# Optimization experiments

Hardware: AMD Instinct MI355X
Metric: run time of the kernel (lower is better)

The kernel has to match this reference:

```python
import jax, jax.numpy as jnp
import numpy as np

T, B, D_IN, D_H, D_OUT = 16, 8192, 512, 1024, 256


def setup_inputs() -> dict:
    key = jax.random.key(0)
    ks = jax.random.split(key, 4)
    # He-style scaled init to keep activations sane
    x = jax.random.normal(ks[0], (B, D_IN), dtype=jnp.float32)
    W1 = jax.random.normal(ks[1], (T, D_IN, D_H), dtype=jnp.float32) / np.sqrt(D_IN)
    b1 = jnp.zeros((T, D_H), dtype=jnp.float32)
    W2 = jax.random.normal(ks[2], (T, D_H, D_H), dtype=jnp.float32) / np.sqrt(D_H)
    b2 = jnp.zeros((T, D_H), dtype=jnp.float32)
    W3 = jax.random.normal(ks[3], (T, D_H, D_OUT), dtype=jnp.float32) / np.sqrt(D_H)
    b3 = jnp.zeros((T, D_OUT), dtype=jnp.float32)
    return {"x": x, "W1": W1, "b1": b1, "W2": W2, "b2": b2, "W3": W3, "b3": b3}


def reference(x, W1, b1, W2, b2, W3, b3):
    # Batched over the tree dimension t: one grouped GEMM per layer instead of
    # a Python loop over trees.
    h = jax.nn.relu(jnp.einsum('bi,tih->tbh', x, W1) + b1[:, None, :])   # [T,B,H]
    h = jax.nn.relu(jnp.einsum('tbh,thk->tbk', h, W2) + b2[:, None, :])  # [T,B,H]
    out = jnp.einsum('tbh,tho->tbo', h, W3) + b3[:, None, :]             # [T,B,O]
    return jnp.mean(out, axis=0)                                          # [B,O]
```

## Files before the change

### kernel.cpp

```cpp
#include <hip/hip_runtime.h>
#include <hip/hip_bf16.h>
#include <stdint.h>

#define T_TREES 16
#define B_ROWS  8192
#define DIN     512
#define DH      1024
#define DOUT    256

typedef unsigned short u16;
typedef __attribute__((ext_vector_type(8))) short short8;
typedef __attribute__((ext_vector_type(16))) float floatx16;

__device__ __forceinline__ u16 f2bf(float f) {
    union { float f; uint32_t u; } v; v.f = f;
    uint32_t u = v.u;
    uint32_t r = (u + 0x7fffu + ((u >> 16) & 1u)) >> 16;
    return (u16)r;
}

__device__ __forceinline__ void async_copy16(const u16* g, u16* l) {
    __builtin_amdgcn_global_load_lds(
        (const __attribute__((address_space(1))) uint32_t*)g,
        (__attribute__((address_space(3))) uint32_t*)l,
        16, 0, 0);
}

__global__ void prep_v9(const float* __restrict__ x, u16* __restrict__ xb,
                        const float* __restrict__ b3, float* __restrict__ out,
                        const float* __restrict__ W1, const float* __restrict__ W2,
                        const float* __restrict__ W3,
                        u16* __restrict__ W1b, u16* __restrict__ W2b,
                        u16* __restrict__ W3b) {
    __shared__ float tile[32][33];
    if (blockIdx.x < 4096) {
        int idx = blockIdx.x * 256 + threadIdx.x;
        float4 v = ((const float4*)x)[idx];
        ushort4 o;
        o.x = f2bf(v.x); o.y = f2bf(v.y); o.z = f2bf(v.z); o.w = f2bf(v.w);
        ((ushort4*)xb)[idx] = o;
    } else if (blockIdx.x < 12288) {
        int idx = (blockIdx.x - 4096) * 256 + threadIdx.x;
        int o = idx & (DOUT - 1);
        float s = 0.f;
#pragma unroll
        for (int t = 0; t < T_TREES; t++) s += b3[t * DOUT + o];
        out[idx] = s * (1.f / T_TREES);
    } else {
        int bid = blockIdx.x - 12288;
        int t = bid / 1792, tl = bid - t * 1792;
        const float* in; u16* outp; int K, N, kt, nt; float scale = 1.f;
        if (tl < 512)       { in = W1; outp = W1b; K = DIN; N = DH;   kt = tl & 15; nt = tl >> 4; }
        else if (tl < 1536) { tl -= 512;  in = W2; outp = W2b; K = DH; N = DH;   kt = tl & 31; nt = tl >> 5; }
        else                { tl -= 1536; in = W3; outp = W3b; K = DH; N = DOUT; kt = tl & 31; nt = tl >> 5;
                              scale = 1.f / T_TREES; }
        int k0 = kt * 32, n0 = nt * 32;
        const float* inb = in + (size_t)t * K * N;
        u16* outb = outp + (size_t)t * K * N;
        int c4 = threadIdx.x & 7, rr = threadIdx.x >> 3;
        float4 v = *(const float4*)&inb[(size_t)(k0 + rr) * N + n0 + c4 * 4];
        tile[rr][c4 * 4 + 0] = v.x;
        tile[rr][c4 * 4 + 1] = v.y;
        tile[rr][c4 * 4 + 2] = v.z;
        tile[rr][c4 * 4 + 3] = v.w;
        __syncthreads();
        if (threadIdx.x < 128) {
            int n  = threadIdx.x >> 2;
            int kq = threadIdx.x & 3;
            short8 o;
#pragma unroll
            for (int j = 0; j < 8; j++)
                ((u16*)&o)[j] = f2bf(tile[kq * 8 + j][n] * scale);
            *(short8*)&outb[(size_t)(n0 + n) * K + k0 + kq * 8] = o;
        }
    }
}

__global__ void reduce_v9(const float* __restrict__ Part, float* __restrict__ Out, int g) {
    int idx = blockIdx.x * 256 + threadIdx.x;
    float4 s = ((const float4*)Out)[idx];
    for (int t = 0; t < g; t++) {
        float4 p = ((const float4*)(Part + (size_t)t * B_ROWS * DOUT))[idx];
        s.x += p.x; s.y += p.y; s.z += p.z; s.w += p.w;
    }
    ((float4*)Out)[idx] = s;
}


#define GEMM_PREAMBLE_COMMON()                               \
    const int tid  = threadIdx.x;                            \
    const int wave = tid >> 6;                               \
    const int lane = tid & 63;                               \
    const int l31  = lane & 31;                              \
    const int h    = lane >> 5;                              \
    const int rg   = tid >> 3;                               \
    const int colE = (((tid & 7) ^ (rg & 7)) << 3);          \
    const int xm   = l31 & 7;

#define STAGE256(kt_, p_)                                                              \
    {                                                                                  \
        const int k0_ = (kt_) * 64;                                                    \
        u16* lA_ = lds + (p_) * 32768 + wave * 512;                                    \
        u16* lB_ = lA_ + 16384;                                                        \
        _Pragma("unroll")                                                              \
        for (int j_ = 0; j_ < 4; j_++) {                                               \
            const int row_ = j_ * 64 + rg;                                             \
            async_copy16(Ab + (size_t)(m0 + row_) * K + k0_ + colE, lA_ + j_ * 4096);  \
            async_copy16(Bb + (size_t)(n0 + row_) * K + k0_ + colE, lB_ + j_ * 4096);  \
        }                                                                              \
    }

#define C256_PASS(A_, B_, mh_)                                                         \
    {                                                                                  \
        short8 afr[2][4];                                                              \
        _Pragma("unroll")                                                              \
        for (int mf = 0; mf < 2; mf++) {                                               \
            const int r_ = wm2 * 128 + (mh_) * 64 + mf * 32 + l31;                     \
            _Pragma("unroll")                                                          \
            for (int kk = 0; kk < 4; kk++)                                             \
                afr[mf][kk] = *(const short8*)&A_[r_ * 64 + (((kk * 2 + h) ^ xm) << 3)]; \
        }                                                                              \
        __builtin_amdgcn_s_setprio(1);                                                 \
        _Pragma("unroll")                                                              \
        for (int kk = 0; kk < 4; kk++)                                                 \
            _Pragma("unroll")                                                          \
            for (int mf = 0; mf < 2; mf++)                                             \
                _Pragma("unroll")                                                      \
                for (int nf = 0; nf < 2; nf++)                                         \
                    acc[(mh_) * 2 + mf][nf] = __builtin_amdgcn_mfma_f32_32x32x16_bf16( \
                        afr[mf][kk], bfr[nf][kk], acc[(mh_) * 2 + mf][nf], 0, 0, 0);   \
        __builtin_amdgcn_s_setprio(0);                                                 \
    }

#define COMPUTE256(p_)                                                                 \
    {                                                                                  \
        const u16* A_ = lds + (p_) * 32768;                                            \
        const u16* B_ = A_ + 16384;                                                    \
        short8 bfr[2][4];                                                              \
        _Pragma("unroll")                                                              \
        for (int nf = 0; nf < 2; nf++) {                                               \
            const int r_ = wn4 * 64 + nf * 32 + l31;                                   \
            _Pragma("unroll")                                                          \
            for (int kk = 0; kk < 4; kk++)                                             \
                bfr[nf][kk] = *(const short8*)&B_[r_ * 64 + (((kk * 2 + h) ^ xm) << 3)]; \
        }                                                                              \
        if (wm2 == 0) { C256_PASS(A_, B_, 0); C256_PASS(A_, B_, 1); }                  \
        else          { C256_PASS(A_, B_, 1); C256_PASS(A_, B_, 0); }                  \
    }

#define GEMM_MAIN(STAGE_, COMPUTE_)                                              \
    STAGE_(0, 0);                                                                \
    STAGE_(1, 1);                                                                \
    for (int kt = 0; kt < NT; kt++) {                                            \
        const int p_ = kt & 1;                                                   \
        if (kt < NT - 1) asm volatile("s_waitcnt vmcnt(8)\n\ts_barrier" ::: "memory"); \
        else             asm volatile("s_waitcnt vmcnt(0)\n\ts_barrier" ::: "memory"); \
        COMPUTE_(p_);                                                            \
        asm volatile("s_barrier" ::: "memory");                                  \
        if (kt + 2 < NT) STAGE_(kt + 2, p_);                                     \
    }

__global__ __launch_bounds__(512, 2)
void gemm_l2_v9(const u16* __restrict__ A, size_t aStrideT,
                const u16* __restrict__ Bt,
                const float* __restrict__ bias,
                u16* __restrict__ C,
                int M, int N, int K) {
    extern __shared__ u16 lds[];

    const int t = blockIdx.z;
    const u16* Ab = A + (size_t)t * aStrideT;
    const u16* Bb = Bt + (size_t)t * (size_t)N * K;
    u16* Cb = C + (size_t)t * (size_t)M * N;
    const float* biasb = bias + (size_t)t * N;

    const int m0 = blockIdx.x * 256;
    const int n0 = blockIdx.y * 256;

    GEMM_PREAMBLE_COMMON();
    const int wm2 = wave >> 2;
    const int wn4 = wave & 3;

    floatx16 acc[4][2];
#pragma unroll
    for (int ai = 0; ai < 4; ai++)
#pragma unroll
        for (int nf = 0; nf < 2; nf++)
#pragma unroll
            for (int r = 0; r < 16; r++) acc[ai][nf][r] = 0.f;

    const int NT = K >> 6;
    GEMM_MAIN(STAGE256, COMPUTE256);

#pragma unroll
    for (int nf = 0; nf < 2; nf++) {
        const int n = n0 + wn4 * 64 + nf * 32 + l31;
        const float bv = biasb[n];
#pragma unroll
        for (int ai = 0; ai < 4; ai++) {
#pragma unroll
            for (int r = 0; r < 16; r++) {
                const int m = m0 + wm2 * 128 + ai * 32 + (r & 3) + 8 * (r >> 2) + 4 * h;
                float v = acc[ai][nf][r] + bv;
                v = v > 0.f ? v : 0.f;
                Cb[(size_t)m * N + n] = f2bf(v);
            }
        }
    }
}

#define STAGE128(kt_, p_)                                                              \
    {                                                                                  \
        const int k0_ = (kt_) * 64;                                                    \
        u16* lA_ = lds + (p_) * 16384 + wave * 512;                                    \
        u16* lB_ = lA_ + 8192;                                                         \
        _Pragma("unroll")                                                              \
        for (int j_ = 0; j_ < 4; j_++) {                                               \
            const int row_ = j_ * 32 + rg;                                             \
            async_copy16(Ab + (size_t)(m0 + row_) * K + k0_ + colE, lA_ + j_ * 2048);  \
            async_copy16(Bb + (size_t)(n0 + row_) * K + k0_ + colE, lB_ + j_ * 2048);  \
        }                                                                              \
    }

#define STAGE_L3(kt_, p_)                                                              \
    {                                                                                  \
        const int lt_ = ltBase + ((kt_) >> 4);                                         \
        const int k0_ = ((kt_) & 15) * 64;                                             \
        const u16* At_ = H2g + (size_t)lt_ * B_ROWS * DH;                              \
        const u16* Bt_ = W3g + (size_t)lt_ * DOUT * DH;                                \
        u16* lA_ = lds + (p_) * 16384 + wave * 512;                                    \
        u16* lB_ = lA_ + 8192;                                                         \
        _Pragma("unroll")                                                              \
        for (int j_ = 0; j_ < 4; j_++) {                                               \
            const int row_ = j_ * 32 + rg;                                             \
            async_copy16(At_ + (size_t)(m0 + row_) * DH + k0_ + colE, lA_ + j_ * 2048);\
            async_copy16(Bt_ + (size_t)(n0 + row_) * DH + k0_ + colE, lB_ + j_ * 2048);\
        }                                                                              \
    }

#define COMPUTE128(p_)                                                                 \
    {                                                                                  \
        const u16* A_ = lds + (p_) * 16384;                                            \
        const u16* B_ = A_ + 8192;                                                     \
        short8 bfr[2][4], afr[2][4];                                                   \
        _Pragma("unroll")                                                              \
        for (int nf = 0; nf < 2; nf++) {                                               \
            const int r_ = wn + nf * 32 + l31;                                         \
            _Pragma("unroll")                                                          \
            for (int kk = 0; kk < 4; kk++)                                             \
                bfr[nf][kk] = *(const short8*)&B_[r_ * 64 + (((kk * 2 + h) ^ xm) << 3)]; \
        }                                                                              \
        _Pragma("unroll")                                                              \
        for (int mf = 0; mf < 2; mf++) {                                               \
            const int r_ = wm + mf * 32 + l31;                                         \
            _Pragma("unroll")                                                          \
            for (int kk = 0; kk < 4; kk++)                                             \
                afr[mf][kk] = *(const short8*)&A_[r_ * 64 + (((kk * 2 + h) ^ xm) << 3)]; \
        }                                                                              \
        __builtin_amdgcn_s_setprio(1);                                                 \
        _Pragma("unroll")                                                              \
        for (int kk = 0; kk < 4; kk++)                                                 \
            _Pragma("unroll")                                                          \
            for (int mf = 0; mf < 2; mf++)                                             \
                _Pragma("unroll")                                                      \
                for (int nf = 0; nf < 2; nf++)                                         \
                    acc[mf][nf] = __builtin_amdgcn_mfma_f32_32x32x16_bf16(             \
                        afr[mf][kk], bfr[nf][kk], acc[mf][nf], 0, 0, 0);               \
        __builtin_amdgcn_s_setprio(0);                                                 \
    }

__global__ __launch_bounds__(256, 2)
void gemm_l1_v9(const u16* __restrict__ A, size_t aStrideT,
                const u16* __restrict__ Bt,
                const float* __restrict__ bias,
                u16* __restrict__ C,
                int M, int N, int K) {
    extern __shared__ u16 lds[];

    const int t = blockIdx.z;
    const u16* Ab = A + (size_t)t * aStrideT;
    const u16* Bb = Bt + (size_t)t * (size_t)N * K;
    u16* Cb = C + (size_t)t * (size_t)M * N;
    const float* biasb = bias + (size_t)t * N;

    const int m0 = blockIdx.x * 128;
    const int n0 = blockIdx.y * 128;

    GEMM_PREAMBLE_COMMON();
    const int wm = (wave >> 1) * 64;
    const int wn = (wave & 1) * 64;

    floatx16 acc[2][2];
#pragma unroll
    for (int mf = 0; mf < 2; mf++)
#pragma unroll
        for (int nf = 0; nf < 2; nf++)
#pragma unroll
            for (int r = 0; r < 16; r++) acc[mf][nf][r] = 0.f;

    const int NT = K >> 6;
    GEMM_MAIN(STAGE128, COMPUTE128);

#pragma unroll
    for (int nf = 0; nf < 2; nf++) {
        const int n = n0 + wn + nf * 32 + l31;
        const float bv = biasb[n];
#pragma unroll
        for (int mf = 0; mf < 2; mf++) {
#pragma unroll
            for (int r = 0; r < 16; r++) {
                const int m = m0 + wm + mf * 32 + (r & 3) + 8 * (r >> 2) + 4 * h;
                float v = acc[mf][nf][r] + bv;
                v = v > 0.f ? v : 0.f;
                Cb[(size_t)m * N + n] = f2bf(v);
            }
        }
    }
}

__global__ __launch_bounds__(256, 2)
void gemm_l3_v9(const u16* __restrict__ H2g, const u16* __restrict__ W3g,
                float* __restrict__ Part, int treesPerBlock) {
    extern __shared__ u16 lds[];

    const int m0 = blockIdx.x * 128;
    const int n0 = blockIdx.y * 128;
    const int ltBase = blockIdx.z * treesPerBlock;
    float* Pb = Part + (size_t)blockIdx.z * B_ROWS * DOUT;

    GEMM_PREAMBLE_COMMON();
    const int wm = (wave >> 1) * 64;
    const int wn = (wave & 1) * 64;

    floatx16 acc[2][2];
#pragma unroll
    for (int mf = 0; mf < 2; mf++)
#pragma unroll
        for (int nf = 0; nf < 2; nf++)
#pragma unroll
            for (int r = 0; r < 16; r++) acc[mf][nf][r] = 0.f;

    const int NT = treesPerBlock << 4;
    GEMM_MAIN(STAGE_L3, COMPUTE128);

#pragma unroll
    for (int nf = 0; nf < 2; nf++) {
        const int n = n0 + wn + nf * 32 + l31;
#pragma unroll
        for (int mf = 0; mf < 2; mf++) {
#pragma unroll
            for (int r = 0; r < 16; r++) {
                const int m = m0 + wm + mf * 32 + (r & 3) + 8 * (r >> 2) + 4 * h;
                Pb[(size_t)m * DOUT + n] = acc[mf][nf][r];
            }
        }
    }
}

extern "C" void kernel_launch(void* const* d_in, const int* in_sizes, int n_in,
                              void* d_out, int out_size, void* d_ws, size_t ws_size,
                              hipStream_t stream) {
    const float* x  = (const float*)d_in[0];
    const float* W1 = (const float*)d_in[1];
    const float* b1 = (const float*)d_in[2];
    const float* W2 = (const float*)d_in[3];
    const float* b2 = (const float*)d_in[4];
    const float* W3 = (const float*)d_in[5];
    const float* b3 = (const float*)d_in[6];
    float* out = (float*)d_out;

    const size_t XB_BYTES = 8388608ull;
    const size_t W1B_BYTES = 16777216ull, W2B_BYTES = 33554432ull, W3B_BYTES = 8388608ull;
    const size_t FIXED = XB_BYTES + W1B_BYTES + W2B_BYTES + W3B_BYTES;
    const size_t PER_TREE = 33554432ull;

    uint8_t* ws = (uint8_t*)d_ws;
    u16* xb  = (u16*)ws;
    u16* W1b = (u16*)(ws + XB_BYTES);
    u16* W2b = (u16*)(ws + XB_BYTES + W1B_BYTES);
    u16* W3b = (u16*)(ws + XB_BYTES + W1B_BYTES + W2B_BYTES);
    u16* h1  = (u16*)(ws + FIXED);
    float* part = (float*)(ws + FIXED);

    int g = 16;
    while (g > 1 && FIXED + (size_t)g * PER_TREE > ws_size) g >>= 1;
    const int nG = T_TREES / g;
    u16* h2 = (u16*)(ws + FIXED + (size_t)g * (PER_TREE / 2));

    prep_v9<<<12288 + 1792 * T_TREES, 256, 0, stream>>>(
        x, xb, b3, out, W1, W2, W3, W1b, W2b, W3b);

    const uint32_t LDS256 = 131072;
    const uint32_t LDS128 = 65536;

    const int tpb = (g >= 2) ? 2 : 1;
    const int zd = g / tpb;

    for (int gi = 0; gi < nG; gi++) {
        const int t0 = gi * g;
        gemm_l1_v9<<<dim3(B_ROWS / 128, DH / 128, g), 256, LDS128, stream>>>(
            xb, 0, W1b + (size_t)t0 * DIN * DH, b1 + (size_t)t0 * DH, h1, B_ROWS, DH, DIN);
        gemm_l2_v9<<<dim3(B_ROWS / 256, DH / 256, g), 512, LDS256, stream>>>(
            h1, (size_t)B_ROWS * DH, W2b + (size_t)t0 * DH * DH, b2 + (size_t)t0 * DH,
            h2, B_ROWS, DH, DH);
        gemm_l3_v9<<<dim3(B_ROWS / 128, DOUT / 128, zd), 256, LDS128, stream>>>(
            h2, W3b + (size_t)t0 * DH * DOUT, part, tpb);
        reduce_v9<<<(B_ROWS * DOUT / 4) / 256, 256, 0, stream>>>(part, out, zd);
    }
}
```

Baseline: 813.7 us.

## Restructure layer-2 GEMM main loop into barrier-synchronized phases per A sub-tile

```diff
diff --git a/kernel.cpp b/kernel.cpp
--- a/kernel.cpp
+++ b/kernel.cpp
@@ -26,12 +26,12 @@
         16, 0, 0);
 }
 
-__global__ void prep_v9(const float* __restrict__ x, u16* __restrict__ xb,
-                        const float* __restrict__ b3, float* __restrict__ out,
-                        const float* __restrict__ W1, const float* __restrict__ W2,
-                        const float* __restrict__ W3,
-                        u16* __restrict__ W1b, u16* __restrict__ W2b,
-                        u16* __restrict__ W3b) {
+__global__ void prep_v10(const float* __restrict__ x, u16* __restrict__ xb,
+                         const float* __restrict__ b3, float* __restrict__ out,
+                         const float* __restrict__ W1, const float* __restrict__ W2,
+                         const float* __restrict__ W3,
+                         u16* __restrict__ W1b, u16* __restrict__ W2b,
+                         u16* __restrict__ W3b) {
     __shared__ float tile[32][33];
     if (blockIdx.x < 4096) {
         int idx = blockIdx.x * 256 + threadIdx.x;
@@ -76,7 +76,7 @@
     }
 }
 
-__global__ void reduce_v9(const float* __restrict__ Part, float* __restrict__ Out, int g) {
+__global__ void reduce_v10(const float* __restrict__ Part, float* __restrict__ Out, int g) {
     int idx = blockIdx.x * 256 + threadIdx.x;
     float4 s = ((const float4*)Out)[idx];
     for (int t = 0; t < g; t++) {
@@ -110,12 +110,163 @@
         }                                                                              \
     }
 
-#define C256_PASS(A_, B_, mh_)                                                         \
+#define C256_PH(A_, ai_)                                                               \
     {                                                                                  \
-        short8 afr[2][4];                                                              \
+        short8 afr[4];                                                                 \
+        const int r_ = wm2 * 128 + (ai_) * 32 + l31;                                   \
+        _Pragma("unroll")                                                              \
+        for (int kk = 0; kk < 4; kk++)                                                 \
+            afr[kk] = *(const short8*)&A_[r_ * 64 + (((kk * 2 + h) ^ xm) << 3)];       \
+        asm volatile("s_barrier" ::: "memory");                                        \
+        __builtin_amdgcn_s_setprio(1);                                                 \
+        _Pragma("unroll")                                                              \
+        for (int kk = 0; kk < 4; kk++)                                                 \
+            _Pragma("unroll")                                                          \
+            for (int nf = 0; nf < 2; nf++)                                             \
+                acc[ai_][nf] = __builtin_amdgcn_mfma_f32_32x32x16_bf16(                \
+                    afr[kk], bfr[nf][kk], acc[ai_][nf], 0, 0, 0);                      \
+        __builtin_amdgcn_s_setprio(0);                                                 \
+    }
+
+#define GEMM256_MAIN_8PH()                                                             \
+    STAGE256(0, 0);                                                                    \
+    STAGE256(1, 1);                                                                    \
+    asm volatile("s_waitcnt vmcnt(8)\n\ts_barrier" ::: "memory");                      \
+    for (int kt = 0; kt < NT; kt++) {                                                  \
+        const int p_ = kt & 1;                                                         \
+        const u16* A_ = lds + p_ * 32768;                                              \
+        const u16* B_ = A_ + 16384;                                                    \
+        short8 bfr[2][4];                                                              \
+        _Pragma("unroll")                                                              \
+        for (int nf = 0; nf < 2; nf++) {                                               \
+            const int r_ = wn4 * 64 + nf * 32 + l31;                                   \
+            _Pragma("unroll")                                                          \
+            for (int kk = 0; kk < 4; kk++)                                             \
+                bfr[nf][kk] = *(const short8*)&B_[r_ * 64 + (((kk * 2 + h) ^ xm) << 3)]; \
+        }                                                                              \
+        C256_PH(A_, 0);                                                                \
+        asm volatile("s_barrier" ::: "memory");                                        \
+        C256_PH(A_, 1);                                                                \
+        asm volatile("s_barrier" ::: "memory");                                        \
+        C256_PH(A_, 2);                                                                \
+        asm volatile("s_barrier" ::: "memory");                                        \
+        {              \
+            short8 afr[4];                                                             \
+            const int r_ = wm2 * 128 + 96 + l31;                                       \
+            _Pragma("unroll")                                                          \
+            for (int kk = 0; kk < 4; kk++)                                             \
+                afr[kk] = *(const short8*)&A_[r_ * 64 + (((kk * 2 + h) ^ xm) << 3)];   \
+            asm volatile("s_barrier" ::: "memory");                                    \
+            __builtin_amdgcn_s_setprio(1);                                             \
+            _Pragma("unroll")                                                          \
+            for (int kk = 0; kk < 4; kk++)                                             \
+                _Pragma("unroll")                                                      \
+                for (int nf = 0; nf < 2; nf++)                                         \
+                    acc[3][nf] = __builtin_amdgcn_mfma_f32_32x32x16_bf16(              \
+                        afr[kk], bfr[nf][kk], acc[3][nf], 0, 0, 0);                    \
+            __builtin_amdgcn_s_setprio(0);                                             \
+            if (kt + 2 < NT) {                                                         \
+                STAGE256(kt + 2, p_);                                                  \
+                asm volatile("s_waitcnt vmcnt(8)\n\ts_barrier" ::: "memory");          \
+            } else {                                                                   \
+                asm volatile("s_waitcnt vmcnt(0)\n\ts_barrier" ::: "memory");          \
+            }                                                                          \
+        }                                                                              \
+    }
+
+__global__ __launch_bounds__(512, 2)
+void gemm_l2_v10(const u16* __restrict__ A, size_t aStrideT,
+                 const u16* __restrict__ Bt,
+                 const float* __restrict__ bias,
+                 u16* __restrict__ C,
+                 int M, int N, int K) {
+    extern __shared__ u16 lds[];
+
+    const int t = blockIdx.z;
+    const u16* Ab = A + (size_t)t * aStrideT;
+    const u16* Bb = Bt + (size_t)t * (size_t)N * K;
+    u16* Cb = C + (size_t)t * (size_t)M * N;
+    const float* biasb = bias + (size_t)t * N;
+
+    const int m0 = blockIdx.x * 256;
+    const int n0 = blockIdx.y * 256;
+
+    GEMM_PREAMBLE_COMMON();
+    const int wm2 = wave >> 2;
+    const int wn4 = wave & 3;
+
+    floatx16 acc[4][2];
+#pragma unroll
+    for (int ai = 0; ai < 4; ai++)
+#pragma unroll
+        for (int nf = 0; nf < 2; nf++)
+#pragma unroll
+            for (int r = 0; r < 16; r++) acc[ai][nf][r] = 0.f;
+
+    const int NT = K >> 6;
+    GEMM256_MAIN_8PH();
+
+#pragma unroll
+    for (int nf = 0; nf < 2; nf++) {
+        const int n = n0 + wn4 * 64 + nf * 32 + l31;
+        const float bv = biasb[n];
+#pragma unroll
+        for (int ai = 0; ai < 4; ai++) {
+#pragma unroll
+            for (int r = 0; r < 16; r++) {
+                const int m = m0 + wm2 * 128 + ai * 32 + (r & 3) + 8 * (r >> 2) + 4 * h;
+                float v = acc[ai][nf][r] + bv;
+                v = v > 0.f ? v : 0.f;
+                Cb[(size_t)m * N + n] = f2bf(v);
+            }
+        }
+    }
+}
+
+#define STAGE128(kt_, p_)                                                              \
+    {                                                                                  \
+        const int k0_ = (kt_) * 64;                                                    \
+        u16* lA_ = lds + (p_) * 16384 + wave * 512;                                    \
+        u16* lB_ = lA_ + 8192;                                                         \
+        _Pragma("unroll")                                                              \
+        for (int j_ = 0; j_ < 4; j_++) {                                               \
+            const int row_ = j_ * 32 + rg;                                             \
+            async_copy16(Ab + (size_t)(m0 + row_) * K + k0_ + colE, lA_ + j_ * 2048);  \
+            async_copy16(Bb + (size_t)(n0 + row_) * K + k0_ + colE, lB_ + j_ * 2048);  \
+        }                                                                              \
+    }
+
+#define STAGE_L3(kt_, p_)                                                              \
+    {                                                                                  \
+        const int lt_ = ltBase + ((kt_) >> 4);                                         \
+        const int k0_ = ((kt_) & 15) * 64;                                             \
+        const u16* At_ = H2g + (size_t)lt_ * B_ROWS * DH;                              \
+        const u16* Bt_ = W3g + (size_t)lt_ * DOUT * DH;                                \
+        u16* lA_ = lds + (p_) * 16384 + wave * 512;                                    \
+        u16* lB_ = lA_ + 8192;                                                         \
+        _Pragma("unroll")                                                              \
+        for (int j_ = 0; j_ < 4; j_++) {                                               \
+            const int row_ = j_ * 32 + rg;                                             \
+            async_copy16(At_ + (size_t)(m0 + row_) * DH + k0_ + colE, lA_ + j_ * 2048);\
+            async_copy16(Bt_ + (size_t)(n0 + row_) * DH + k0_ + colE, lB_ + j_ * 2048);\
+        }                                                                              \
+    }
+
+#define COMPUTE128(p_)                                                                 \
+    {                                                                                  \
+        const u16* A_ = lds + (p_) * 16384;                                            \
+        const u16* B_ = A_ + 8192;                                                     \
+        short8 bfr[2][4], afr[2][4];                                                   \
+        _Pragma("unroll")                                                              \
+        for (int nf = 0; nf < 2; nf++) {                                               \
+            const int r_ = wn + nf * 32 + l31;                                         \
+            _Pragma("unroll")                                                          \
+            for (int kk = 0; kk < 4; kk++)                                             \
+                bfr[nf][kk] = *(const short8*)&B_[r_ * 64 + (((kk * 2 + h) ^ xm) << 3)]; \
+        }                                                                              \
         _Pragma("unroll")                                                              \
         for (int mf = 0; mf < 2; mf++) {                                               \
-            const int r_ = wm2 * 128 + (mh_) * 64 + mf * 32 + l31;                     \
+            const int r_ = wm + mf * 32 + l31;                                         \
             _Pragma("unroll")                                                          \
             for (int kk = 0; kk < 4; kk++)                                             \
                 afr[mf][kk] = *(const short8*)&A_[r_ * 64 + (((kk * 2 + h) ^ xm) << 3)]; \
@@ -127,25 +278,9 @@
             for (int mf = 0; mf < 2; mf++)                                             \
                 _Pragma("unroll")                                                      \
                 for (int nf = 0; nf < 2; nf++)                                         \
-                    acc[(mh_) * 2 + mf][nf] = __builtin_amdgcn_mfma_f32_32x32x16_bf16( \
-                        afr[mf][kk], bfr[nf][kk], acc[(mh_) * 2 + mf][nf], 0, 0, 0);   \
+                    acc[mf][nf] = __builtin_amdgcn_mfma_f32_32x32x16_bf16(             \
+                        afr[mf][kk], bfr[nf][kk], acc[mf][nf], 0, 0, 0);               \
         __builtin_amdgcn_s_setprio(0);                                                 \
-    }
-
-#define COMPUTE256(p_)                                                                 \
-    {                                                                                  \
-        const u16* A_ = lds + (p_) * 32768;                                            \
-        const u16* B_ = A_ + 16384;                                                    \
-        short8 bfr[2][4];                                                              \
-        _Pragma("unroll")                                                              \
-        for (int nf = 0; nf < 2; nf++) {                                               \
-            const int r_ = wn4 * 64 + nf * 32 + l31;                                   \
-            _Pragma("unroll")                                                          \
-            for (int kk = 0; kk < 4; kk++)                                             \
-                bfr[nf][kk] = *(const short8*)&B_[r_ * 64 + (((kk * 2 + h) ^ xm) << 3)]; \
-        }                                                                              \
-        if (wm2 == 0) { C256_PASS(A_, B_, 0); C256_PASS(A_, B_, 1); }                  \
-        else          { C256_PASS(A_, B_, 1); C256_PASS(A_, B_, 0); }                  \
     }
 
 #define GEMM_MAIN(STAGE_, COMPUTE_)                                              \
@@ -160,121 +295,12 @@
         if (kt + 2 < NT) STAGE_(kt + 2, p_);                                     \
     }
 
-__global__ __launch_bounds__(512, 2)
-void gemm_l2_v9(const u16* __restrict__ A, size_t aStrideT,
-                const u16* __restrict__ Bt,
-                const float* __restrict__ bias,
-                u16* __restrict__ C,
-                int M, int N, int K) {
-    extern __shared__ u16 lds[];
-
-    const int t = blockIdx.z;
-    const u16* Ab = A + (size_t)t * aStrideT;
-    const u16* Bb = Bt + (size_t)t * (size_t)N * K;
-    u16* Cb = C + (size_t)t * (size_t)M * N;
-    const float* biasb = bias + (size_t)t * N;
-
-    const int m0 = blockIdx.x * 256;
-    const int n0 = blockIdx.y * 256;
-
-    GEMM_PREAMBLE_COMMON();
-    const int wm2 = wave >> 2;
-    const int wn4 = wave & 3;
-
-    floatx16 acc[4][2];
-#pragma unroll
-    for (int ai = 0; ai < 4; ai++)
-#pragma unroll
-        for (int nf = 0; nf < 2; nf++)
-#pragma unroll
-            for (int r = 0; r < 16; r++) acc[ai][nf][r] = 0.f;
-
-    const int NT = K >> 6;
-    GEMM_MAIN(STAGE256, COMPUTE256);
-
-#pragma unroll
-    for (int nf = 0; nf < 2; nf++) {
-        const int n = n0 + wn4 * 64 + nf * 32 + l31;
-        const float bv = biasb[n];
-#pragma unroll
-        for (int ai = 0; ai < 4; ai++) {
-#pragma unroll
-            for (int r = 0; r < 16; r++) {
-                const int m = m0 + wm2 * 128 + ai * 32 + (r & 3) + 8 * (r >> 2) + 4 * h;
-                float v = acc[ai][nf][r] + bv;
-                v = v > 0.f ? v : 0.f;
-                Cb[(size_t)m * N + n] = f2bf(v);
-            }
-        }
-    }
-}
-
-#define STAGE128(kt_, p_)                                                              \
-    {                                                                                  \
-        const int k0_ = (kt_) * 64;                                                    \
-        u16* lA_ = lds + (p_) * 16384 + wave * 512;                                    \
-        u16* lB_ = lA_ + 8192;                                                         \
-        _Pragma("unroll")                                                              \
-        for (int j_ = 0; j_ < 4; j_++) {                                               \
-            const int row_ = j_ * 32 + rg;                                             \
-            async_copy16(Ab + (size_t)(m0 + row_) * K + k0_ + colE, lA_ + j_ * 2048);  \
-            async_copy16(Bb + (size_t)(n0 + row_) * K + k0_ + colE, lB_ + j_ * 2048);  \
-        }                                                                              \
-    }
-
-#define STAGE_L3(kt_, p_)                                                              \
-    {                                                                                  \
-        const int lt_ = ltBase + ((kt_) >> 4);                                         \
-        const int k0_ = ((kt_) & 15) * 64;                                             \
-        const u16* At_ = H2g + (size_t)lt_ * B_ROWS * DH;                              \
-        const u16* Bt_ = W3g + (size_t)lt_ * DOUT * DH;                                \
-        u16* lA_ = lds + (p_) * 16384 + wave * 512;                                    \
-        u16* lB_ = lA_ + 8192;                                                         \
-        _Pragma("unroll")                                                              \
-        for (int j_ = 0; j_ < 4; j_++) {                                               \
-            const int row_ = j_ * 32 + rg;                                             \
-            async_copy16(At_ + (size_t)(m0 + row_) * DH + k0_ + colE, lA_ + j_ * 2048);\
-            async_copy16(Bt_ + (size_t)(n0 + row_) * DH + k0_ + colE, lB_ + j_ * 2048);\
-        }                                                                              \
-    }
-
-#define COMPUTE128(p_)                                                                 \
-    {                                                                                  \
-        const u16* A_ = lds + (p_) * 16384;                                            \
-        const u16* B_ = A_ + 8192;                                                     \
-        short8 bfr[2][4], afr[2][4];                                                   \
-        _Pragma("unroll")                                                              \
-        for (int nf = 0; nf < 2; nf++) {                                               \
-            const int r_ = wn + nf * 32 + l31;                                         \
-            _Pragma("unroll")                                                          \
-            for (int kk = 0; kk < 4; kk++)                                             \
-                bfr[nf][kk] = *(const short8*)&B_[r_ * 64 + (((kk * 2 + h) ^ xm) << 3)]; \
-        }                                                                              \
-        _Pragma("unroll")                                                              \
-        for (int mf = 0; mf < 2; mf++) {                                               \
-            const int r_ = wm + mf * 32 + l31;                                         \
-            _Pragma("unroll")                                                          \
-            for (int kk = 0; kk < 4; kk++)                                             \
-                afr[mf][kk] = *(const short8*)&A_[r_ * 64 + (((kk * 2 + h) ^ xm) << 3)]; \
-        }                                                                              \
-        __builtin_amdgcn_s_setprio(1);                                                 \
-        _Pragma("unroll")                                                              \
-        for (int kk = 0; kk < 4; kk++)                                                 \
-            _Pragma("unroll")                                                          \
-            for (int mf = 0; mf < 2; mf++)                                             \
-                _Pragma("unroll")                                                      \
-                for (int nf = 0; nf < 2; nf++)                                         \
-                    acc[mf][nf] = __builtin_amdgcn_mfma_f32_32x32x16_bf16(             \
-                        afr[mf][kk], bfr[nf][kk], acc[mf][nf], 0, 0, 0);               \
-        __builtin_amdgcn_s_setprio(0);                                                 \
-    }
-
 __global__ __launch_bounds__(256, 2)
-void gemm_l1_v9(const u16* __restrict__ A, size_t aStrideT,
-                const u16* __restrict__ Bt,
-                const float* __restrict__ bias,
-                u16* __restrict__ C,
-                int M, int N, int K) {
+void gemm_l1_v10(const u16* __restrict__ A, size_t aStrideT,
+                 const u16* __restrict__ Bt,
+                 const float* __restrict__ bias,
+                 u16* __restrict__ C,
+                 int M, int N, int K) {
     extern __shared__ u16 lds[];
 
     const int t = blockIdx.z;
@@ -319,8 +345,8 @@
 }
 
 __global__ __launch_bounds__(256, 2)
-void gemm_l3_v9(const u16* __restrict__ H2g, const u16* __restrict__ W3g,
-                float* __restrict__ Part, int treesPerBlock) {
+void gemm_l3_v10(const u16* __restrict__ H2g, const u16* __restrict__ W3g,
+                 float* __restrict__ Part, int treesPerBlock) {
     extern __shared__ u16 lds[];
 
     const int m0 = blockIdx.x * 128;
@@ -387,7 +413,7 @@
     const int nG = T_TREES / g;
     u16* h2 = (u16*)(ws + FIXED + (size_t)g * (PER_TREE / 2));
 
-    prep_v9<<<12288 + 1792 * T_TREES, 256, 0, stream>>>(
+    prep_v10<<<12288 + 1792 * T_TREES, 256, 0, stream>>>(
         x, xb, b3, out, W1, W2, W3, W1b, W2b, W3b);
 
     const uint32_t LDS256 = 131072;
@@ -398,13 +424,13 @@
 
     for (int gi = 0; gi < nG; gi++) {
         const int t0 = gi * g;
-        gemm_l1_v9<<<dim3(B_ROWS / 128, DH / 128, g), 256, LDS128, stream>>>(
+        gemm_l1_v10<<<dim3(B_ROWS / 128, DH / 128, g), 256, LDS128, stream>>>(
             xb, 0, W1b + (size_t)t0 * DIN * DH, b1 + (size_t)t0 * DH, h1, B_ROWS, DH, DIN);
-        gemm_l2_v9<<<dim3(B_ROWS / 256, DH / 256, g), 512, LDS256, stream>>>(
+        gemm_l2_v10<<<dim3(B_ROWS / 256, DH / 256, g), 512, LDS256, stream>>>(
             h1, (size_t)B_ROWS * DH, W2b + (size_t)t0 * DH * DH, b2 + (size_t)t0 * DH,
             h2, B_ROWS, DH, DH);
-        gemm_l3_v9<<<dim3(B_ROWS / 128, DOUT / 128, zd), 256, LDS128, stream>>>(
+        gemm_l3_v10<<<dim3(B_ROWS / 128, DOUT / 128, zd), 256, LDS128, stream>>>(
             h2, W3b + (size_t)t0 * DH * DOUT, part, tpb);
-        reduce_v9<<<(B_ROWS * DOUT / 4) / 256, 256, 0, stream>>>(part, out, zd);
-    }
-}
+        reduce_v10<<<(B_ROWS * DOUT / 4) / 256, 256, 0, stream>>>(part, out, zd);
+    }
+}
```

Result: no change. 807.9 us (-0.7%).
